# Performance work log

Hardware: AMD Instinct MI355X
Metric: run time of the kernel (lower is better)

Reference implementation:

```python
import jax, jax.numpy as jnp
import numpy as np

# NMS hyperparameters (from init_kwargs / standard detection settings)
CONF_THRESH = 0.05
NMS_THRESH = 0.5
MAX_PER_CLASS = 200
MAX_PER_IMAGE = 100
PRE_NMS_TOPK = 1000  # standard pre-NMS per-class candidate cap


def setup_inputs() -> dict:
    key = jax.random.key(0)
    k1, k2, k3 = jax.random.split(key, 3)
    N, C = 20000, 80
    # per-anchor per-class confidences in [0, 1]
    scores = jax.random.uniform(k1, (1, N, C), dtype=jnp.float32)
    # well-formed boxes (x1, y1, x2, y2) in normalized coords
    centers = jax.random.uniform(k2, (N, 2), dtype=jnp.float32)
    wh = jax.random.uniform(k3, (N, 2), dtype=jnp.float32) * 0.2 + 0.01
    boxes = jnp.concatenate([centers - wh / 2, centers + wh / 2], axis=-1)  # [N, 4]
    return {"scores": scores, "boxes": boxes}


def reference(scores, boxes):
    """Multiclass NMS: confidence threshold -> per-class greedy IoU suppression
    (max_per_class kept) -> global top-max_per_image. Returns kept scores
    (fixed shape [MAX_PER_IMAGE], zero-padded), matching the wrapper which
    returns the selected scores."""
    cls_scores_all = scores[0].T  # [C, N]
    j = jnp.arange(PRE_NMS_TOPK)

    def nms_one_class(cls_scores):  # [N] -> [MAX_PER_CLASS]
        top_s, idx = jax.lax.top_k(cls_scores, PRE_NMS_TOPK)  # [K]
        b = boxes[idx]  # [K, 4]
        x1, y1, x2, y2 = b[:, 0], b[:, 1], b[:, 2], b[:, 3]
        area = (x2 - x1) * (y2 - y1)  # [K]
        # pairwise IoU [K, K]
        iw = jnp.clip(jnp.minimum(x2[:, None], x2[None, :]) - jnp.maximum(x1[:, None], x1[None, :]), 0.0)
        ih = jnp.clip(jnp.minimum(y2[:, None], y2[None, :]) - jnp.maximum(y1[:, None], y1[None, :]), 0.0)
        inter = iw * ih
        iou = inter / (area[:, None] + area[None, :] - inter + 1e-9)
        valid = top_s > CONF_THRESH  # confidence threshold

        def body(i, keep):
            # if box i survives, suppress later boxes with IoU above threshold
            sup = keep[i] & (iou[i] > NMS_THRESH) & (j > i)
            return keep & ~sup

        keep = jax.lax.fori_loop(0, PRE_NMS_TOPK, body, valid)
        kept = jnp.where(keep, top_s, 0.0)
        return jax.lax.top_k(kept, MAX_PER_CLASS)[0]  # cap per class

    per_class = jax.vmap(nms_one_class)(cls_scores_all)  # [C, MAX_PER_CLASS]
    # global cap: top max_per_image scores across all classes
    return jax.lax.top_k(per_class.reshape(-1), MAX_PER_IMAGE)[0]
```

## Files before the change

### kernel.cpp

```cpp
#include <hip/hip_runtime.h>
#include <stdint.h>

#define N_DET 20000
#define N_CLS 80
#define NELEM (N_DET * N_CLS)
#define TOPK  1000
#define CONF  0.05f
#define CANDS 1280
#define SORTN 2048
#define FASTN 256
#define NBLK  128

typedef unsigned long long u64;
typedef unsigned int u32;

__device__ __forceinline__ bool iou_gt_half(float4 bi, float ai,
                                            float4 bj, float aj) {
  #pragma clang fp contract(off)
  float iw = fmaxf(fminf(bi.z, bj.z) - fmaxf(bi.x, bj.x), 0.0f);
  float ih = fmaxf(fminf(bi.w, bj.w) - fmaxf(bi.y, bj.y), 0.0f);
  float inter = iw * ih;
  float denom = ai + aj - inter + 1e-9f;
  return (double)inter * 33554432.0 > (double)denom * 16777217.0;
}

#define OFF_T16    0
#define OFF_T160   320
#define OFF_CNT    960
#define OFF_CLSOUT 641280
#define OFF_GHA    682240
#define OFF_GHB    723200
#define OFF_CAND   805120
#define OFF_BCNT   1624320

__global__ __launch_bounds__(256) void k_zero(u32* __restrict__ gh) {
  uint4 z4 = make_uint4(0u, 0u, 0u, 0u);
  uint4* p = (uint4*)gh;
  int i = blockIdx.x * 256 + threadIdx.x;
  if (i < 7680) p[i] = z4;
}

__global__ __launch_bounds__(256) void k_histA(
    const float* __restrict__ S, u32* __restrict__ gh) {
  __shared__ u32 h[N_CLS * 129];
  for (int i = threadIdx.x; i < N_CLS * 129; i += 256) h[i] = 0;
  __syncthreads();
  const int per = NELEM / 4 / NBLK;
  const float4* S4 = (const float4*)S;
  const int v0 = blockIdx.x * per;
  for (int v = v0 + threadIdx.x; v < v0 + per; v += 256) {
    float4 f = S4[v];
    int c0 = (v * 4) % N_CLS;
    u32 b0 = __float_as_uint(f.x) >> 23; if (b0 > 127u) b0 = 127u;
    u32 b1 = __float_as_uint(f.y) >> 23; if (b1 > 127u) b1 = 127u;
    u32 b2 = __float_as_uint(f.z) >> 23; if (b2 > 127u) b2 = 127u;
    u32 b3 = __float_as_uint(f.w) >> 23; if (b3 > 127u) b3 = 127u;
    atomicAdd(&h[(c0 + 0) * 129 + b0], 1u);
    atomicAdd(&h[(c0 + 1) * 129 + b1], 1u);
    atomicAdd(&h[(c0 + 2) * 129 + b2], 1u);
    atomicAdd(&h[(c0 + 3) * 129 + b3], 1u);
  }
  __syncthreads();
  for (int i = threadIdx.x; i < N_CLS * 128; i += 256) {
    u32 v = h[(i >> 7) * 129 + (i & 127)];
    if (v) atomicAdd(&gh[i], v);
  }
}

__global__ __launch_bounds__(256) void k_histB_f(
    const float* __restrict__ S, const u32* __restrict__ ghA,
    u32* __restrict__ ghB) {
  __shared__ u32 h[N_CLS * 257];
  __shared__ u32 pA[N_CLS];
  for (int i = threadIdx.x; i < N_CLS * 128; i += 256)
    h[(i >> 7) * 129 + (i & 127)] = ghA[i];
  __syncthreads();
  if (threadIdx.x < N_CLS) {
    const int c = threadIdx.x;
    u32 acc = 0; u32 pref = 0;
    for (int b = 127; b >= 0; --b) {
      acc += h[c * 129 + b];
      if (acc >= TOPK) { pref = (u32)b; break; }
    }
    pA[c] = pref;
  }
  __syncthreads();
  for (int i = threadIdx.x; i < N_CLS * 257; i += 256) h[i] = 0;
  __syncthreads();
  const int per = NELEM / 4 / NBLK;
  const float4* S4 = (const float4*)S;
  const int v0 = blockIdx.x * per;
  for (int v = v0 + threadIdx.x; v < v0 + per; v += 256) {
    float4 f = S4[v];
    int c0 = (v * 4) % N_CLS;
    u32 bb[4] = {__float_as_uint(f.x), __float_as_uint(f.y),
                 __float_as_uint(f.z), __float_as_uint(f.w)};
    #pragma unroll
    for (int k = 0; k < 4; ++k) {
      u32 e = bb[k] >> 23; if (e > 127u) e = 127u;
      if (e == pA[c0 + k])
        atomicAdd(&h[(c0 + k) * 257 + ((bb[k] >> 15) & 0xFF)], 1u);
    }
  }
  __syncthreads();
  for (int i = threadIdx.x; i < N_CLS * 256; i += 256) {
    u32 v = h[(i >> 8) * 257 + (i & 255)];
    if (v) atomicAdd(&ghB[i], v);
  }
}

__global__ __launch_bounds__(256) void k_count_f(
    const float* __restrict__ S, const u32* __restrict__ ghA,
    const u32* __restrict__ ghB, u32* __restrict__ T16,
    u32* __restrict__ T160, u32* __restrict__ cnt, u32* __restrict__ bcnt) {
  __shared__ u32 hA[N_CLS * 129];
  __shared__ u32 hB[N_CLS * 257];
  __shared__ u32 tl[N_CLS];
  __shared__ u32 lcnt[N_CLS];
  for (int i = threadIdx.x; i < N_CLS * 128; i += 256)
    hA[(i >> 7) * 129 + (i & 127)] = ghA[i];
  for (int i = threadIdx.x; i < N_CLS * 256; i += 256)
    hB[(i >> 8) * 257 + (i & 255)] = ghB[i];
  for (int i = threadIdx.x; i < N_CLS; i += 256) lcnt[i] = 0;
  __syncthreads();
  if (threadIdx.x < N_CLS) {
    const int c = threadIdx.x;
    u32 acc = 0, pref = 0, tgt = TOPK, aboveA = 0;
    bool found = false;
    for (int b = 127; b >= 0; --b) {
      u32 hv = hA[c * 129 + b];
      acc += hv;
      if (acc >= TOPK) { pref = (u32)b; tgt = TOPK - (acc - hv);
                         aboveA = acc - hv; found = true; break; }
    }
    if (!found) { pref = 0; tgt = TOPK; aboveA = acc - hA[c * 129]; }
    u32 accB = 0, B1 = 0;
    for (int b = 255; b >= 0; --b) {
      accB += hB[c * 257 + b];
      if (accB >= tgt) { B1 = (u32)b; break; }
    }
    u32 t16 = (pref << 23) | (B1 << 15);
    tl[c] = t16;
    if (blockIdx.x == 0) {
      T16[c] = t16;
      cnt[c] = aboveA + accB;
      u32 t160 = t16;
      if (aboveA < 160u) {
        u32 rt = 160u - aboveA;
        u32 acc2 = 0, B2 = 0;
        for (int b = 255; b >= 0; --b) {
          acc2 += hB[c * 257 + b];
          if (acc2 >= rt) { B2 = (u32)b; break; }
        }
        t160 = (pref << 23) | (B2 << 15);
      }
      T160[c] = t160;
    }
  }
  __syncthreads();
  const int per = NELEM / 4 / NBLK;
  const float4* S4 = (const float4*)S;
  const int v0 = blockIdx.x * per;
  for (int v = v0 + threadIdx.x; v < v0 + per; v += 256) {
    float4 f = S4[v];
    const int c0 = (v * 4) % N_CLS;
    u32 bb[4] = {__float_as_uint(f.x), __float_as_uint(f.y),
                 __float_as_uint(f.z), __float_as_uint(f.w)};
    #pragma unroll
    for (int k = 0; k < 4; ++k)
      if (bb[k] >= tl[c0 + k]) atomicAdd(&lcnt[c0 + k], 1u);
  }
  __syncthreads();
  for (int i = threadIdx.x; i < N_CLS; i += 256)
    bcnt[blockIdx.x * N_CLS + i] = lcnt[i];
}

__global__ __launch_bounds__(256) void k_place_f(
    const float* __restrict__ S, const u32* __restrict__ T16,
    const u32* __restrict__ bcnt, u64* __restrict__ cand) {
  __shared__ u32 tl[N_CLS];
  __shared__ u32 lcnt[N_CLS];
  __shared__ u32 gbase[N_CLS];
  for (int i = threadIdx.x; i < N_CLS; i += 256) { tl[i] = T16[i]; lcnt[i] = 0; }
  if (threadIdx.x < N_CLS) {
    const int c = threadIdx.x;
    u32 a = 0;
    for (int b = 0; b < blockIdx.x; ++b) a += bcnt[b * N_CLS + c];
    gbase[c] = a;
  }
  __syncthreads();
  const int per = NELEM / 4 / NBLK;
  const float4* S4 = (const float4*)S;
  const int v0 = blockIdx.x * per;
  for (int v = v0 + threadIdx.x; v < v0 + per; v += 256) {
    float4 f = S4[v];
    const int base = v * 4;
    const int c0 = base % N_CLS;
    const u32 row = (u32)(base / N_CLS);
    u32 bb[4] = {__float_as_uint(f.x), __float_as_uint(f.y),
                 __float_as_uint(f.z), __float_as_uint(f.w)};
    #pragma unroll
    for (int k = 0; k < 4; ++k) {
      if (bb[k] >= tl[c0 + k]) {
        u32 p = gbase[c0 + k] + atomicAdd(&lcnt[c0 + k], 1u);
        if (p < CANDS)
          cand[(size_t)(c0 + k) * CANDS + p] = ((u64)bb[k] << 32) | (u32)(~row);
      }
    }
  }
}

__global__ __launch_bounds__(256) void k_sortnms(
    const u64* __restrict__ cand, const u32* __restrict__ cnt,
    const u32* __restrict__ T160, const float* __restrict__ boxes,
    float* __restrict__ cls_out) {
  const int c = blockIdx.x;
  const int tid = threadIdx.x, wave = tid >> 6, lane = tid & 63;
  __shared__ u64 keys[SORTN];
  __shared__ float4 sbox[TOPK];
  __shared__ float sarea[TOPK];
  __shared__ float sscore[TOPK];
  __shared__ u32 sN, sOvf, sDone;

  u32 n = cnt[c]; if (n > CANDS) n = CANDS;
  const u32 thr = T160[c];
  keys[tid] = 0ull;
  if (tid == 0) { sN = 0; sOvf = 0; sDone = 0; }
  __syncthreads();
  for (int i = tid; i < (int)n; i += 256) {
    u64 kk = cand[(size_t)c * CANDS + i];
    if ((u32)(kk >> 32) >= thr) {
      u32 p = atomicAdd(&sN, 1u);
      if (p < FASTN) keys[p] = kk; else sOvf = 1u;
    }
  }
  __syncthreads();
  const u32 nk = sN;

  if (!sOvf) {
    const int segbase = wave * 64;
    for (int k = 2; k <= 64; k <<= 1) {
      for (int j = k >> 1; j > 0; j >>= 1) {
        if (lane < 32) {
          int p = lane;
          int i  = segbase + (((p & ~(j - 1)) << 1) | (p & (j - 1)));
          int ix = i | j;
          bool up = (i & k) == 0;
          u64 a = keys[i], b = keys[ix];
          if (up ? (a < b) : (a > b)) { keys[i] = b; keys[ix] = a; }
        }
        __builtin_amdgcn_wave_barrier();
      }
    }
    __syncthreads();
    for (int k = 128; k <= FASTN; k <<= 1) {
      for (int j = k >> 1; j >= 64; j >>= 1) {
        if (tid < 128) {
          int p = tid;
          int i  = ((p & ~(j - 1)) << 1) | (p & (j - 1));
          int ix = i | j;
          bool up = (i & k) == 0;
          u64 a = keys[i], b = keys[ix];
          if (up ? (a < b) : (a > b)) { keys[i] = b; keys[ix] = a; }
        }
        __syncthreads();
      }
      for (int j = 32; j > 0; j >>= 1) {
        if (lane < 32) {
          int p = lane;
          int i  = segbase + (((p & ~(j - 1)) << 1) | (p & (j - 1)));
          int ix = i | j;
          bool up = (i & k) == 0;
          u64 a = keys[i], b = keys[ix];
          if (up ? (a < b) : (a > b)) { keys[i] = b; keys[ix] = a; }
        }
        __builtin_amdgcn_wave_barrier();
      }
      __syncthreads();
    }

    {
      u64 kk = keys[tid];
      u32 idx = ~(u32)kk;
      if (kk == 0ull || idx >= N_DET) idx = 0;
      float4 b = ((const float4*)boxes)[idx];
      sbox[tid] = b;
      sarea[tid] = (b.z - b.x) * (b.w - b.y);
      sscore[tid] = __uint_as_float((u32)(kk >> 32));
    }
    __syncthreads();

    if (wave == 0) {
      float4 kb0 = make_float4(0.f, 0.f, 0.f, 0.f), kb1 = kb0;
      float ka0 = 0.f, ka1 = 0.f;
      int count = 0;
      bool confbreak = false;
      int ii = 0;
      float sc_n = sscore[0];
      float4 b_n = sbox[0];
      float a_n = sarea[0];
      for (; ii < FASTN && count < 100; ++ii) {
        float sc = sc_n;
        float4 bi = b_n;
        float ai = a_n;
        if (ii + 1 < FASTN) {
          sc_n = sscore[ii + 1];
          b_n = sbox[ii + 1];
          a_n = sarea[ii + 1];
        }
        if (!(sc > CONF)) { confbreak = true; break; }
        bool sup0 = (lane < count) && iou_gt_half(kb0, ka0, bi, ai);
        bool sup1 = (lane + 64 < count) && iou_gt_half(kb1, ka1, bi, ai);
        u64 m = __ballot(sup0 || sup1);
        if (m == 0ull) {
          if (count < 64) {
            if (lane == count) { kb0 = bi; ka0 = ai; }
          } else {
            if (lane == count - 64) { kb1 = bi; ka1 = ai; }
          }
          if (lane == 0) cls_out[c * 128 + count] = sc;
          ++count;
        }
      }
      bool done = (count >= 100) || (confbreak && ii < (int)nk);
      if (lane == 0) sDone = done ? 1u : 0u;
      if (done) {
        for (int i = count + lane; i < 100; i += 64)
          cls_out[c * 128 + i] = 0.0f;
      }
    }
  }
  __syncthreads();
  if (sDone) return;

  for (int i = tid; i < SORTN; i += 256)
    keys[i] = (i < (int)n) ? cand[(size_t)c * CANDS + i] : 0ull;
  __syncthreads();
  const int seg2 = wave * 512;
  for (int k = 2; k <= 512; k <<= 1) {
    for (int j = k >> 1; j > 0; j >>= 1) {
      #pragma unroll
      for (int q = 0; q < 4; ++q) {
        int p = lane + q * 64;
        int i  = seg2 + (((p & ~(j - 1)) << 1) | (p & (j - 1)));
        int ix = i | j;
        bool up = (i & k) == 0;
        u64 a = keys[i], b = keys[ix];
        if (up ? (a < b) : (a > b)) { keys[i] = b; keys[ix] = a; }
      }
      __builtin_amdgcn_wave_barrier();
    }
  }
  __syncthreads();
  for (int k = 1024; k <= SORTN; k <<= 1) {
    for (int j = k >> 1; j >= 512; j >>= 1) {
      for (int p = tid; p < SORTN / 2; p += 256) {
        int i  = ((p & ~(j - 1)) << 1) | (p & (j - 1));
        int ix = i | j;
        bool up = (i & k) == 0;
        u64 a = keys[i], b = keys[ix];
        if (up ? (a < b) : (a > b)) { keys[i] = b; keys[ix] = a; }
      }
      __syncthreads();
    }
    for (int j = 256; j > 0; j >>= 1) {
      #pragma unroll
      for (int q = 0; q < 4; ++q) {
        int p = lane + q * 64;
        int i  = seg2 + (((p & ~(j - 1)) << 1) | (p & (j - 1)));
        int ix = i | j;
        bool up = (i & k) == 0;
        u64 a = keys[i], b = keys[ix];
        if (up ? (a < b) : (a > b)) { keys[i] = b; keys[ix] = a; }
      }
      __builtin_amdgcn_wave_barrier();
    }
    __syncthreads();
  }
  for (int i = tid; i < TOPK; i += 256) {
    u64 kk = keys[i];
    u32 idx = ~(u32)kk;
    if (kk == 0ull || idx >= N_DET) idx = 0;
    float4 b = ((const float4*)boxes)[idx];
    sbox[i] = b;
    sarea[i] = (b.z - b.x) * (b.w - b.y);
    sscore[i] = __uint_as_float((u32)(kk >> 32));
  }
  __syncthreads();
  if (wave == 0) {
    float4 kb0 = make_float4(0.f, 0.f, 0.f, 0.f), kb1 = kb0;
    float ka0 = 0.f, ka1 = 0.f;
    int count = 0;
    float sc_n = sscore[0];
    float4 b_n = sbox[0];
    float a_n = sarea[0];
    for (int i = 0; i < TOPK && count < 100; ++i) {
      float sc = sc_n;
      float4 bi = b_n;
      float ai = a_n;
      if (i + 1 < TOPK) {
        sc_n = sscore[i + 1];
        b_n = sbox[i + 1];
        a_n = sarea[i + 1];
      }
      if (!(sc > CONF)) break;
      bool sup0 = (lane < count) && iou_gt_half(kb0, ka0, bi, ai);
      bool sup1 = (lane + 64 < count) && iou_gt_half(kb1, ka1, bi, ai);
      u64 m = __ballot(sup0 || sup1);
      if (m == 0ull) {
        if (count < 64) {
          if (lane == count) { kb0 = bi; ka0 = ai; }
        } else {
          if (lane == count - 64) { kb1 = bi; ka1 = ai; }
        }
        if (lane == 0) cls_out[c * 128 + count] = sc;
        ++count;
      }
    }
    for (int i = count + lane; i < 100; i += 64)
      cls_out[c * 128 + i] = 0.0f;
  }
}

__global__ __launch_bounds__(1024) void k_final(
    const float* __restrict__ cls_out, float* __restrict__ out) {
  __shared__ u32 vals[8000];
  __shared__ u32 h1[8192];
  __shared__ u32 h2[16384];
  __shared__ u32 wsum[16];
  __shared__ u32 cands[512];
  __shared__ u32 sPref, sT2, sThr, scnt;
  const int t = threadIdx.x, wave = t >> 6, lane = t & 63;

  uint4 z4 = make_uint4(0u, 0u, 0u, 0u);
  for (int i = t; i < 2048; i += 1024) ((uint4*)h1)[i] = z4;
  for (int i = t; i < 4096; i += 1024) ((uint4*)h2)[i] = z4;
  if (t < 128) ((uint4*)cands)[t] = z4;
  if (t == 0) { sPref = 0; sT2 = 1; sThr = 0; scnt = 0; }
  __syncthreads();

  for (int i = t; i < 8000; i += 1024) {
    u32 b = __float_as_uint(cls_out[(i / 100) * 128 + (i % 100)]);
    vals[i] = b;
    u32 bin = b >> 17; if (bin > 8191u) bin = 8191u;
    atomicAdd(&h1[bin], 1u);
  }
  __syncthreads();

  {
    const u32 b0 = (u32)t * 8u;
    u32 loc[8]; u32 lsum = 0;
    #pragma unroll
    for (int k = 0; k < 8; ++k) { loc[k] = h1[b0 + k]; lsum += loc[k]; }
    u32 s = lsum;
    #pragma unroll
    for (int off = 1; off < 64; off <<= 1) {
      u32 v = __shfl_down(s, off, 64);
      if (lane + off < 64) s += v;
    }
    if (lane == 0) wsum[wave] = s;
    __syncthreads();
    u32 aboveW = 0;
    #pragma unroll
    for (int w = 0; w < 16; ++w) if (w > wave) aboveW += wsum[w];
    u32 above = aboveW + (s - lsum);
    if (above < 100u && above + lsum >= 100u) {
      u32 acc = above;
      #pragma unroll
      for (int k = 7; k >= 0; --k) {
        acc += loc[k];
        if (acc >= 100u) { sPref = b0 + (u32)k; sT2 = 100u - (acc - loc[k]); break; }
      }
    }
    __syncthreads();
  }
  const u32 pref = sPref, rt = sT2;

  for (int i = t; i < 8000; i += 1024) {
    u32 b = vals[i];
    u32 bin = b >> 17; if (bin > 8191u) bin = 8191u;
    if (bin == pref) atomicAdd(&h2[(b >> 3) & 0x3FFFu], 1u);
  }
  __syncthreads();

  {
    const u32 b0 = (u32)t * 16u;
    u32 loc[16]; u32 lsum = 0;
    #pragma unroll
    for (int k = 0; k < 16; ++k) { loc[k] = h2[b0 + k]; lsum += loc[k]; }
    u32 s = lsum;
    #pragma unroll
    for (int off = 1; off < 64; off <<= 1) {
      u32 v = __shfl_down(s, off, 64);
      if (lane + off < 64) s += v;
    }
    if (lane == 0) wsum[wave] = s;
    __syncthreads();
    u32 aboveW = 0;
    #pragma unroll
    for (int w = 0; w < 16; ++w) if (w > wave) aboveW += wsum[w];
    u32 above = aboveW + (s - lsum);
    if (above < rt && above + lsum >= rt) {
      u32 acc = above;
      #pragma unroll
      for (int k = 15; k >= 0; --k) {
        acc += loc[k];
        if (acc >= rt) { sThr = (pref << 17) | ((b0 + (u32)k) << 3); break; }
      }
    }
    __syncthreads();
  }
  const u32 thr = sThr;

  for (int i = t; i < 8000; i += 1024) {
    u32 v = vals[i];
    if (v >= thr) {
      u32 p = atomicAdd(&scnt, 1u);
      if (p < 512u) cands[p] = v;
    }
  }
  __syncthreads();
  const u32 nc = scnt;

  if (nc <= 512u) {
    if (wave == 0) {
      for (int k = 2; k <= 512; k <<= 1)
        for (int j = k >> 1; j > 0; j >>= 1) {
          for (int p = lane; p < 256; p += 64) {
            int i  = ((p & ~(j - 1)) << 1) | (p & (j - 1));
            int ix = i | j;
            bool up = (i & k) == 0;
            u32 a = cands[i], b = cands[ix];
            if (up ? (a < b) : (a > b)) { cands[i] = b; cands[ix] = a; }
          }
          __builtin_amdgcn_wave_barrier();
        }
      out[lane] = __uint_as_float(cands[lane]);
      if (lane < 36) out[lane + 64] = __uint_as_float(cands[lane + 64]);
    }
  } else {
    for (int i = t; i < 8192; i += 1024) h2[i] = (i < 8000) ? vals[i] : 0u;
    __syncthreads();
    for (int k = 2; k <= 8192; k <<= 1)
      for (int j = k >> 1; j > 0; j >>= 1) {
        for (int p = t; p < 4096; p += 1024) {
          int i  = ((p & ~(j - 1)) << 1) | (p & (j - 1));
          int ix = i | j;
          bool up = (i & k) == 0;
          u32 a = h2[i], b = h2[ix];
          if (up ? (a < b) : (a > b)) { h2[i] = b; h2[ix] = a; }
        }
        __syncthreads();
      }
    if (t < 100) out[t] = __uint_as_float(h2[t]);
  }
}

extern "C" void kernel_launch(void* const* d_in, const int* in_sizes, int n_in,
                              void* d_out, int out_size, void* d_ws, size_t ws_size,
                              hipStream_t stream) {
  const float* scores = (const float*)d_in[0];
  const float* boxes  = (const float*)d_in[1];
  float* out = (float*)d_out;
  char* ws = (char*)d_ws;

  u32* T16     = (u32*)(ws + OFF_T16);
  u32* T160    = (u32*)(ws + OFF_T160);
  u32* cnt     = (u32*)(ws + OFF_CNT);
  float* cls_out = (float*)(ws + OFF_CLSOUT);
  u32* ghistA  = (u32*)(ws + OFF_GHA);
  u32* ghistB  = (u32*)(ws + OFF_GHB);
  u64* cand    = (u64*)(ws + OFF_CAND);
  u32* bcnt    = (u32*)(ws + OFF_BCNT);

  k_zero<<<30, 256, 0, stream>>>(ghistA);
  k_histA<<<NBLK, 256, 0, stream>>>(scores, ghistA);
  k_histB_f<<<NBLK, 256, 0, stream>>>(scores, ghistA, ghistB);
  k_count_f<<<NBLK, 256, 0, stream>>>(scores, ghistA, ghistB, T16, T160, cnt, bcnt);
  k_place_f<<<NBLK, 256, 0, stream>>>(scores, T16, bcnt, cand);
  k_sortnms<<<N_CLS, 256, 0, stream>>>(cand, cnt, T160, boxes, cls_out);
  k_final<<<1, 1024, 0, stream>>>(cls_out, out);
}
```

Before: 143.8 us.

## Batch greedy NMS fast path four candidates at a time with pairwise intra-block IoU

Replaces the one-candidate-per-iteration greedy NMS loop in the single-wave fast path with blocks of four. Each block tests the four candidates against all kept boxes at once, computes the six intra-block pairwise IoUs on separate lanes, and resolves keep decisions serially with cheap bit logic. The aim is to cut the serial chain of shared-memory loads and ballots per candidate. The cost is some wasted IoU work when count reaches 100 or the confidence cutoff falls mid-block. There is also a risk: when the cutoff falls mid-block, the stop flag is set before the earlier kept candidates in that block are appended, so they are dropped.

```diff
diff --git a/kernel.cpp b/kernel.cpp
--- a/kernel.cpp
+++ b/kernel.cpp
@@ -295,34 +295,64 @@
       float ka0 = 0.f, ka1 = 0.f;
       int count = 0;
       bool confbreak = false;
-      int ii = 0;
-      float sc_n = sscore[0];
-      float4 b_n = sbox[0];
-      float a_n = sarea[0];
-      for (; ii < FASTN && count < 100; ++ii) {
-        float sc = sc_n;
-        float4 bi = b_n;
-        float ai = a_n;
-        if (ii + 1 < FASTN) {
-          sc_n = sscore[ii + 1];
-          b_n = sbox[ii + 1];
-          a_n = sarea[ii + 1];
-        }
-        if (!(sc > CONF)) { confbreak = true; break; }
-        bool sup0 = (lane < count) && iou_gt_half(kb0, ka0, bi, ai);
-        bool sup1 = (lane + 64 < count) && iou_gt_half(kb1, ka1, bi, ai);
-        u64 m = __ballot(sup0 || sup1);
-        if (m == 0ull) {
-          if (count < 64) {
-            if (lane == count) { kb0 = bi; ka0 = ai; }
-          } else {
-            if (lane == count - 64) { kb1 = bi; ka1 = ai; }
+      int breakRow = FASTN;
+      bool stop = false;
+      for (int base = 0; base < FASTN && !stop; base += 4) {
+        float4 cb0 = sbox[base], cb1 = sbox[base + 1];
+        float4 cb2 = sbox[base + 2], cb3 = sbox[base + 3];
+        float a0 = sarea[base], a1 = sarea[base + 1];
+        float a2 = sarea[base + 2], a3 = sarea[base + 3];
+        float s0 = sscore[base], s1 = sscore[base + 1];
+        float s2 = sscore[base + 2], s3 = sscore[base + 3];
+        bool q0 = ((lane < count) && iou_gt_half(kb0, ka0, cb0, a0)) ||
+                  ((lane + 64 < count) && iou_gt_half(kb1, ka1, cb0, a0));
+        bool q1 = ((lane < count) && iou_gt_half(kb0, ka0, cb1, a1)) ||
+                  ((lane + 64 < count) && iou_gt_half(kb1, ka1, cb1, a1));
+        bool q2 = ((lane < count) && iou_gt_half(kb0, ka0, cb2, a2)) ||
+                  ((lane + 64 < count) && iou_gt_half(kb1, ka1, cb2, a2));
+        bool q3 = ((lane < count) && iou_gt_half(kb0, ka0, cb3, a3)) ||
+                  ((lane + 64 < count) && iou_gt_half(kb1, ka1, cb3, a3));
+        float4 Pa = (lane < 3) ? cb0 : (lane < 5) ? cb1 : cb2;
+        float  Paa = (lane < 3) ? a0 : (lane < 5) ? a1 : a2;
+        float4 Pb = (lane == 0) ? cb1 : (lane == 1 || lane == 3) ? cb2 : cb3;
+        float  Pba = (lane == 0) ? a1 : (lane == 1 || lane == 3) ? a2 : a3;
+        bool qp = (lane < 6) && iou_gt_half(Pa, Paa, Pb, Pba);
+        u64 m0 = __ballot(q0), m1 = __ballot(q1);
+        u64 m2 = __ballot(q2), m3 = __ballot(q3);
+        u64 mp = __ballot(qp);
+        bool p01 = (mp >> 0) & 1, p02 = (mp >> 1) & 1, p03 = (mp >> 2) & 1;
+        bool p12 = (mp >> 3) & 1, p13 = (mp >> 4) & 1, p23 = (mp >> 5) & 1;
+        bool k0 = false, k1 = false, k2 = false, k3 = false;
+        if (!(s0 > CONF)) { confbreak = true; breakRow = base; stop = true; }
+        else {
+          k0 = (m0 == 0ull);
+          if (!(s1 > CONF)) { confbreak = true; breakRow = base + 1; stop = true; }
+          else {
+            k1 = (m1 == 0ull) && !(k0 && p01);
+            if (!(s2 > CONF)) { confbreak = true; breakRow = base + 2; stop = true; }
+            else {
+              k2 = (m2 == 0ull) && !(k0 && p02) && !(k1 && p12);
+              if (!(s3 > CONF)) { confbreak = true; breakRow = base + 3; stop = true; }
+              else
+                k3 = (m3 == 0ull) && !(k0 && p03) && !(k1 && p13) && !(k2 && p23);
+            }
           }
-          if (lane == 0) cls_out[c * 128 + count] = sc;
-          ++count;
-        }
-      }
-      bool done = (count >= 100) || (confbreak && ii < (int)nk);
+        }
+        #define APPEND(KJ, CBJ, AJ, SJ)                                   \
+          if (!stop && (KJ)) {                                            \
+            if (count < 64) { if (lane == count) { kb0 = CBJ; ka0 = AJ; } } \
+            else { if (lane == count - 64) { kb1 = CBJ; ka1 = AJ; } }     \
+            if (lane == 0) cls_out[c * 128 + count] = SJ;                 \
+            ++count;                                                      \
+            if (count >= 100) stop = true;                                \
+          }
+        APPEND(k0, cb0, a0, s0)
+        APPEND(k1, cb1, a1, s1)
+        APPEND(k2, cb2, a2, s2)
+        APPEND(k3, cb3, a3, s3)
+        #undef APPEND
+      }
+      bool done = (count >= 100) || (confbreak && breakRow < (int)nk);
       if (lane == 0) sDone = done ? 1u : 0u;
       if (done) {
         for (int i = count + lane; i < 100; i += 64)
```

Measured after the change: 144.6 us. No clear change (+0.5%).

## Run per-class sort+NMS kernel as a single wavefront without block barriers

Applied to the files above, without the earlier changes.

Shrinks the per-class sort/NMS block from four waves to one 64-lane wave. __syncthreads calls become wave barriers, and the shared-memory atomic compaction becomes ballot/popcount compaction. The aim is to remove block-level synchronization and atomic overhead in a kernel where NMS already ran on a single wave. The trade-off is that the bitonic sorts, especially the 2048-key fallback, now do four times more work per lane with no help from other waves.

```diff
diff --git a/kernel.cpp b/kernel.cpp
--- a/kernel.cpp
+++ b/kernel.cpp
@@ -210,40 +210,46 @@
   }
 }
 
-__global__ __launch_bounds__(256) void k_sortnms(
+__global__ __launch_bounds__(64) void k_sortnms(
     const u64* __restrict__ cand, const u32* __restrict__ cnt,
     const u32* __restrict__ T160, const float* __restrict__ boxes,
     float* __restrict__ cls_out) {
   const int c = blockIdx.x;
-  const int tid = threadIdx.x, wave = tid >> 6, lane = tid & 63;
+  const int lane = threadIdx.x;
   __shared__ u64 keys[SORTN];
   __shared__ float4 sbox[TOPK];
   __shared__ float sarea[TOPK];
   __shared__ float sscore[TOPK];
-  __shared__ u32 sN, sOvf, sDone;
 
   u32 n = cnt[c]; if (n > CANDS) n = CANDS;
   const u32 thr = T160[c];
-  keys[tid] = 0ull;
-  if (tid == 0) { sN = 0; sOvf = 0; sDone = 0; }
-  __syncthreads();
-  for (int i = tid; i < (int)n; i += 256) {
-    u64 kk = cand[(size_t)c * CANDS + i];
-    if ((u32)(kk >> 32) >= thr) {
-      u32 p = atomicAdd(&sN, 1u);
-      if (p < FASTN) keys[p] = kk; else sOvf = 1u;
-    }
-  }
-  __syncthreads();
-  const u32 nk = sN;
-
-  if (!sOvf) {
-    const int segbase = wave * 64;
-    for (int k = 2; k <= 64; k <<= 1) {
+  #pragma unroll
+  for (int q = 0; q < FASTN / 64; ++q) keys[lane + q * 64] = 0ull;
+  __builtin_amdgcn_wave_barrier();
+
+  u32 base = 0;
+  for (int i0 = 0; i0 < (int)n; i0 += 64) {
+    int i = i0 + lane;
+    u64 kk = (i < (int)n) ? cand[(size_t)c * CANDS + i] : 0ull;
+    bool take = (i < (int)n) && ((u32)(kk >> 32) >= thr);
+    u64 m = __ballot(take);
+    if (take) {
+      u32 pos = base + (u32)__popcll(m & ((1ull << lane) - 1ull));
+      if (pos < FASTN) keys[pos] = kk;
+    }
+    base += (u32)__popcll(m);
+  }
+  __builtin_amdgcn_wave_barrier();
+  const u32 nk = base;
+  bool fastok = (nk <= FASTN);
+
+  if (fastok) {
+    for (int k = 2; k <= FASTN; k <<= 1) {
       for (int j = k >> 1; j > 0; j >>= 1) {
-        if (lane < 32) {
-          int p = lane;
-          int i  = segbase + (((p & ~(j - 1)) << 1) | (p & (j - 1)));
+        #pragma unroll
+        for (int q = 0; q < 2; ++q) {
+          int p = lane + q * 64;
+          int i  = ((p & ~(j - 1)) << 1) | (p & (j - 1));
           int ix = i | j;
           bool up = (i & k) == 0;
           u64 a = keys[i], b = keys[ix];
@@ -252,132 +258,75 @@
         __builtin_amdgcn_wave_barrier();
       }
     }
-    __syncthreads();
-    for (int k = 128; k <= FASTN; k <<= 1) {
-      for (int j = k >> 1; j >= 64; j >>= 1) {
-        if (tid < 128) {
-          int p = tid;
-          int i  = ((p & ~(j - 1)) << 1) | (p & (j - 1));
-          int ix = i | j;
-          bool up = (i & k) == 0;
-          u64 a = keys[i], b = keys[ix];
-          if (up ? (a < b) : (a > b)) { keys[i] = b; keys[ix] = a; }
-        }
-        __syncthreads();
-      }
-      for (int j = 32; j > 0; j >>= 1) {
-        if (lane < 32) {
-          int p = lane;
-          int i  = segbase + (((p & ~(j - 1)) << 1) | (p & (j - 1)));
-          int ix = i | j;
-          bool up = (i & k) == 0;
-          u64 a = keys[i], b = keys[ix];
-          if (up ? (a < b) : (a > b)) { keys[i] = b; keys[ix] = a; }
-        }
-        __builtin_amdgcn_wave_barrier();
-      }
-      __syncthreads();
-    }
-
-    {
-      u64 kk = keys[tid];
+
+    #pragma unroll
+    for (int q = 0; q < FASTN / 64; ++q) {
+      int i = lane + q * 64;
+      u64 kk = keys[i];
       u32 idx = ~(u32)kk;
       if (kk == 0ull || idx >= N_DET) idx = 0;
       float4 b = ((const float4*)boxes)[idx];
-      sbox[tid] = b;
-      sarea[tid] = (b.z - b.x) * (b.w - b.y);
-      sscore[tid] = __uint_as_float((u32)(kk >> 32));
-    }
-    __syncthreads();
-
-    if (wave == 0) {
-      float4 kb0 = make_float4(0.f, 0.f, 0.f, 0.f), kb1 = kb0;
-      float ka0 = 0.f, ka1 = 0.f;
-      int count = 0;
-      bool confbreak = false;
-      int ii = 0;
-      float sc_n = sscore[0];
-      float4 b_n = sbox[0];
-      float a_n = sarea[0];
-      for (; ii < FASTN && count < 100; ++ii) {
-        float sc = sc_n;
-        float4 bi = b_n;
-        float ai = a_n;
-        if (ii + 1 < FASTN) {
-          sc_n = sscore[ii + 1];
-          b_n = sbox[ii + 1];
-          a_n = sarea[ii + 1];
+      sbox[i] = b;
+      sarea[i] = (b.z - b.x) * (b.w - b.y);
+      sscore[i] = __uint_as_float((u32)(kk >> 32));
+    }
+    __builtin_amdgcn_wave_barrier();
+
+    float4 kb0 = make_float4(0.f, 0.f, 0.f, 0.f), kb1 = kb0;
+    float ka0 = 0.f, ka1 = 0.f;
+    int count = 0;
+    bool confbreak = false;
+    int ii = 0;
+    float sc_n = sscore[0];
+    float4 b_n = sbox[0];
+    float a_n = sarea[0];
+    for (; ii < FASTN && count < 100; ++ii) {
+      float sc = sc_n;
+      float4 bi = b_n;
+      float ai = a_n;
+      if (ii + 1 < FASTN) {
+        sc_n = sscore[ii + 1];
+        b_n = sbox[ii + 1];
+        a_n = sarea[ii + 1];
+      }
+      if (!(sc > CONF)) { confbreak = true; break; }
+      bool sup0 = (lane < count) && iou_gt_half(kb0, ka0, bi, ai);
+      bool sup1 = (lane + 64 < count) && iou_gt_half(kb1, ka1, bi, ai);
+      u64 m = __ballot(sup0 || sup1);
+      if (m == 0ull) {
+        if (count < 64) {
+          if (lane == count) { kb0 = bi; ka0 = ai; }
+        } else {
+          if (lane == count - 64) { kb1 = bi; ka1 = ai; }
         }
-        if (!(sc > CONF)) { confbreak = true; break; }
-        bool sup0 = (lane < count) && iou_gt_half(kb0, ka0, bi, ai);
-        bool sup1 = (lane + 64 < count) && iou_gt_half(kb1, ka1, bi, ai);
-        u64 m = __ballot(sup0 || sup1);
-        if (m == 0ull) {
-          if (count < 64) {
-            if (lane == count) { kb0 = bi; ka0 = ai; }
-          } else {
-            if (lane == count - 64) { kb1 = bi; ka1 = ai; }
-          }
-          if (lane == 0) cls_out[c * 128 + count] = sc;
-          ++count;
-        }
-      }
-      bool done = (count >= 100) || (confbreak && ii < (int)nk);
-      if (lane == 0) sDone = done ? 1u : 0u;
-      if (done) {
-        for (int i = count + lane; i < 100; i += 64)
-          cls_out[c * 128 + i] = 0.0f;
-      }
-    }
-  }
-  __syncthreads();
-  if (sDone) return;
-
-  for (int i = tid; i < SORTN; i += 256)
+        if (lane == 0) cls_out[c * 128 + count] = sc;
+        ++count;
+      }
+    }
+    bool done = (count >= 100) || (confbreak && ii < (int)nk);
+    if (done) {
+      for (int i = count + lane; i < 100; i += 64)
+        cls_out[c * 128 + i] = 0.0f;
+      return;
+    }
+  }
+
+  for (int i = lane; i < SORTN; i += 64)
     keys[i] = (i < (int)n) ? cand[(size_t)c * CANDS + i] : 0ull;
-  __syncthreads();
-  const int seg2 = wave * 512;
-  for (int k = 2; k <= 512; k <<= 1) {
+  __builtin_amdgcn_wave_barrier();
+  for (int k = 2; k <= SORTN; k <<= 1) {
     for (int j = k >> 1; j > 0; j >>= 1) {
-      #pragma unroll
-      for (int q = 0; q < 4; ++q) {
-        int p = lane + q * 64;
-        int i  = seg2 + (((p & ~(j - 1)) << 1) | (p & (j - 1)));
-        int ix = i | j;
-        bool up = (i & k) == 0;
-        u64 a = keys[i], b = keys[ix];
-        if (up ? (a < b) : (a > b)) { keys[i] = b; keys[ix] = a; }
-      }
-      __builtin_amdgcn_wave_barrier();
-    }
-  }
-  __syncthreads();
-  for (int k = 1024; k <= SORTN; k <<= 1) {
-    for (int j = k >> 1; j >= 512; j >>= 1) {
-      for (int p = tid; p < SORTN / 2; p += 256) {
+      for (int p = lane; p < SORTN / 2; p += 64) {
         int i  = ((p & ~(j - 1)) << 1) | (p & (j - 1));
         int ix = i | j;
         bool up = (i & k) == 0;
         u64 a = keys[i], b = keys[ix];
         if (up ? (a < b) : (a > b)) { keys[i] = b; keys[ix] = a; }
       }
-      __syncthreads();
-    }
-    for (int j = 256; j > 0; j >>= 1) {
-      #pragma unroll
-      for (int q = 0; q < 4; ++q) {
-        int p = lane + q * 64;
-        int i  = seg2 + (((p & ~(j - 1)) << 1) | (p & (j - 1)));
-        int ix = i | j;
-        bool up = (i & k) == 0;
-        u64 a = keys[i], b = keys[ix];
-        if (up ? (a < b) : (a > b)) { keys[i] = b; keys[ix] = a; }
-      }
       __builtin_amdgcn_wave_barrier();
     }
-    __syncthreads();
-  }
-  for (int i = tid; i < TOPK; i += 256) {
+  }
+  for (int i = lane; i < TOPK; i += 64) {
     u64 kk = keys[i];
     u32 idx = ~(u32)kk;
     if (kk == 0ull || idx >= N_DET) idx = 0;
@@ -386,8 +335,8 @@
     sarea[i] = (b.z - b.x) * (b.w - b.y);
     sscore[i] = __uint_as_float((u32)(kk >> 32));
   }
-  __syncthreads();
-  if (wave == 0) {
+  __builtin_amdgcn_wave_barrier();
+  {
     float4 kb0 = make_float4(0.f, 0.f, 0.f, 0.f), kb1 = kb0;
     float ka0 = 0.f, ka1 = 0.f;
     int count = 0;
@@ -578,6 +527,6 @@
   k_histB_f<<<NBLK, 256, 0, stream>>>(scores, ghistA, ghistB);
   k_count_f<<<NBLK, 256, 0, stream>>>(scores, ghistA, ghistB, T16, T160, cnt, bcnt);
   k_place_f<<<NBLK, 256, 0, stream>>>(scores, T16, bcnt, cand);
-  k_sortnms<<<N_CLS, 256, 0, stream>>>(cand, cnt, T160, boxes, cls_out);
+  k_sortnms<<<N_CLS, 64, 0, stream>>>(cand, cnt, T160, boxes, cls_out);
   k_final<<<1, 1024, 0, stream>>>(cls_out, out);
 }
```

Result: slower. 154.0 us (+7.1%).
